# Optimization experiments

Hardware: AMD Instinct MI355X
Metric: run time of the kernel (lower is better)

## Reference

```python
import jax, jax.numpy as jnp
import numpy as np

V, C, H, W, RM, RD = 16, 16, 1024, 1024, 8, 4


def _cpx(x):
    # last dim 2 = (real, imag) -> complex64
    return jax.lax.complex(x[..., 0], x[..., 1])


def setup_inputs() -> dict:
    key = jax.random.key(0)
    ks = jax.random.split(key, 12)
    rn = lambda k, s, sc=1.0: jax.random.normal(k, s, dtype=jnp.float32) * sc
    ASYM = 0.01
    exp_init = jnp.array([2.0, 0.0], dtype=jnp.float32)  # exponents_initial_value_(real,imag)
    return {
        "base": rn(ks[0], (H, W, 2)),
        "mod_u": rn(ks[1], (C, H, RM, 2), 0.35),
        "mod_v": rn(ks[2], (C, RM, W, 2), 0.35),
        "del_u": rn(ks[3], (C, H, RD, 2), 0.35),
        "del_v": rn(ks[4], (C, RD, W, 2), 0.35),
        "exp_base": exp_init + rn(ks[5], (2,), ASYM),
        "exp_mod": exp_init[None, :] + rn(ks[6], (C, 2), ASYM),
        "exp_del": exp_init[None, :] + rn(ks[7], (C, 2), ASYM),
        "bias": rn(ks[8], (C, 2)),
        "scale": rn(ks[9], (C, 2)),
        "coef": rn(ks[10], (V, C, 2)),  # uniform(-2,2) real + small imag in torch; randn ok for baseline
    }


def reference(base, mod_u, mod_v, del_u, del_v, exp_base, exp_mod, exp_del, bias, scale, coef):
    b = _cpx(base)  # [H, W] complex64
    # low-rank complex reconstructions: [C, H, W]
    mod = jnp.einsum('chr,crw->chw', _cpx(mod_u), _cpx(mod_v))
    dlt = jnp.einsum('chr,crw->chw', _cpx(del_u), _cpx(del_v))
    # trainable complex exponentiation: z**w = exp(w * log z)
    pb = jnp.exp(_cpx(exp_base) * jnp.log(b))                        # [H, W]
    pm = jnp.exp(_cpx(exp_mod)[:, None, None] * jnp.log(mod))       # [C, H, W]
    pd = jnp.exp(_cpx(exp_del)[:, None, None] * jnp.log(dlt))       # [C, H, W]
    comp = _cpx(scale)[:, None, None] * (pb[None] * pm + pd) + _cpx(bias)[:, None, None]
    # coefficient-weighted sum over C components -> [V, H, W] (avoids [V,C,H,W] materialization)
    out = jnp.einsum('vc,chw->vhw', _cpx(coef), comp)
    return jnp.stack([out.real, out.imag], axis=-1)  # [V, H, W, 2] float32
```

## Files before the change

kernel.cpp:

```cpp
#include <hip/hip_runtime.h>
#include <stdint.h>

#define NV 16
#define NC 16
#define NH 1024
#define NW 1024
#define NRM 8
#define NRD 4

typedef __attribute__((ext_vector_type(4))) _Float16 f16x4;
typedef __attribute__((ext_vector_type(2))) __fp16 fp16x2_raw;
typedef __attribute__((ext_vector_type(4))) float f32x4;

#define MFMA16(a, b, c) __builtin_amdgcn_mfma_f32_16x16x16f16((a), (b), (c), 0, 0, 0)

struct cfloat { float x, y; };

__device__ __forceinline__ uint32_t pkh(float a, float b) {
    fp16x2_raw h = __builtin_amdgcn_cvt_pkrtz(a, b);
    return __builtin_bit_cast(uint32_t, h);
}

__device__ __forceinline__ f16x4 mk4(uint32_t lo, uint32_t hi) {
    union { uint32_t u[2]; f16x4 v; } t;
    t.u[0] = lo; t.u[1] = hi;
    return t.v;
}

__device__ __forceinline__ float fast_atan2f(float y, float x) {
    float ax = fabsf(x), ay = fabsf(y);
    float mx = fmaxf(ax, ay), mn = fminf(ax, ay);
    float a = __fdividef(mn, mx);
    float s = a * a;
    float p =              -0.01172120f;
    p = fmaf(p, s,  0.05265332f);
    p = fmaf(p, s, -0.11643287f);
    p = fmaf(p, s,  0.19354346f);
    p = fmaf(p, s, -0.33262347f);
    p = fmaf(p, s,  0.99997726f);
    p = p * a;
    float t = (ay > ax) ? (1.57079632679f - p) : p;
    t = (x < 0.0f) ? (3.14159265359f - t) : t;
    return (y < 0.0f) ? -t : t;
}

__device__ __forceinline__ cfloat cpow_(float zr, float zi, float wr, float wi) {
    float L  = 0.5f * __logf(fmaf(zr, zr, zi * zi));
    float th = fast_atan2f(zi, zr);
    float er = fmaf(wr, L,  -wi * th);
    float ei = fmaf(wr, th,  wi * L);
    float m  = __expf(er);
    float sv, cv;
    __sincosf(ei, &sv, &cv);
    cfloat r; r.x = m * cv; r.y = m * sv; return r;
}

#define CMAC(AR, AI, BR, BI) do { \
    tr_ = fmaf((AR), (BR), fmaf(-(AI), (BI), tr_)); \
    ti_ = fmaf((AR), (BI), fmaf( (AI), (BR), ti_)); } while (0)

__global__ __launch_bounds__(256)
void transpose_v(const float* __restrict__ mod_v, const float* __restrict__ del_v,
                 float* __restrict__ mvT, float* __restrict__ dvT)
{
    const int idx = blockIdx.x * 256 + threadIdx.x;
    const int c = idx >> 10, w = idx & 1023;
    float2* mt = reinterpret_cast<float2*>(mvT) + idx * NRM;
    const float2* ms = reinterpret_cast<const float2*>(mod_v) + c * NRM * NW + w;
    #pragma unroll
    for (int r = 0; r < NRM; ++r) mt[r] = ms[r * NW];
    float2* dt = reinterpret_cast<float2*>(dvT) + idx * NRD;
    const float2* dsrc = reinterpret_cast<const float2*>(del_v) + c * NRD * NW + w;
    #pragma unroll
    for (int r = 0; r < NRD; ++r) dt[r] = dsrc[r * NW];
}

struct V6 { float4 m0, m1, m2, m3, d0, d1; };

template <bool TR>
__device__ __forceinline__ V6 load_v(const float* __restrict__ mvT, const float* __restrict__ dvT,
                                     const float* __restrict__ mod_v, const float* __restrict__ del_v,
                                     int c, int w)
{
    V6 r;
    if (TR) {
        const float4* mp = reinterpret_cast<const float4*>(mvT) + (c * NW + w) * 4;
        r.m0 = mp[0]; r.m1 = mp[1]; r.m2 = mp[2]; r.m3 = mp[3];
        const float4* dp = reinterpret_cast<const float4*>(dvT) + (c * NW + w) * 2;
        r.d0 = dp[0]; r.d1 = dp[1];
    } else {
        const float2* m = reinterpret_cast<const float2*>(mod_v) + c * NRM * NW + w;
        float2 a0 = m[0], a1 = m[NW], a2 = m[2*NW], a3 = m[3*NW];
        float2 a4 = m[4*NW], a5 = m[5*NW], a6 = m[6*NW], a7 = m[7*NW];
        r.m0 = make_float4(a0.x, a0.y, a1.x, a1.y);
        r.m1 = make_float4(a2.x, a2.y, a3.x, a3.y);
        r.m2 = make_float4(a4.x, a4.y, a5.x, a5.y);
        r.m3 = make_float4(a6.x, a6.y, a7.x, a7.y);
        const float2* d = reinterpret_cast<const float2*>(del_v) + c * NRD * NW + w;
        float2 b0 = d[0], b1 = d[NW], b2 = d[2*NW], b3 = d[3*NW];
        r.d0 = make_float4(b0.x, b0.y, b1.x, b1.y);
        r.d1 = make_float4(b2.x, b2.y, b3.x, b3.y);
    }
    return r;
}

template <bool TR>
__global__ __launch_bounds__(256)
void fused_kernel(const float* __restrict__ base, const float* __restrict__ mod_u,
                  const float* __restrict__ mod_v, const float* __restrict__ del_u,
                  const float* __restrict__ del_v, const float* __restrict__ exp_base,
                  const float* __restrict__ exp_mod, const float* __restrict__ exp_del,
                  const float* __restrict__ bias_, const float* __restrict__ scale_,
                  const float* __restrict__ coef, float* __restrict__ out,
                  const float* __restrict__ mvT, const float* __restrict__ dvT)
{
    __shared__ uint32_t lds[8192];
    __shared__ float4 uA4[NC][2][4];
    __shared__ float4 uD4[NC][2][2];

    const int tid    = threadIdx.x;
    const int lane   = tid & 63;
    const int wv     = tid >> 6;
    const int wchunk = (int)(blockIdx.x & 3);
    const int hp     = (int)(blockIdx.x >> 2);
    const int w      = (wchunk << 8) | tid;
    const int h0     = hp * 2;
    const int wbase  = (wchunk << 8) | (wv << 6);

    {
        float* uAf = reinterpret_cast<float*>(uA4);
        float* uDf = reinterpret_cast<float*>(uD4);
        int i = tid;
        {
            const int c = i >> 5, rr = (i >> 4) & 1, e = i & 15;
            uAf[i] = mod_u[((c * NH) + (h0 + rr)) * (NRM * 2) + e];
        }
        i = tid + 256;
        {
            const int c = i >> 5, rr = (i >> 4) & 1, e = i & 15;
            uAf[i] = mod_u[((c * NH) + (h0 + rr)) * (NRM * 2) + e];
        }
        if (tid < 256) {
            const int c = tid >> 4, rr = (tid >> 3) & 1, e = tid & 7;
            uDf[tid] = del_u[((c * NH) + (h0 + rr)) * (NRD * 2) + e];
        }
    }
    __syncthreads();

    const int vv = lane & 15;
    const int c0 = (lane >> 4) << 2;

    const float4 cfa = *reinterpret_cast<const float4*>(coef   + (vv * NC + c0) * 2);
    const float4 cfb = *reinterpret_cast<const float4*>(coef   + (vv * NC + c0) * 2 + 4);
    const float4 sca = *reinterpret_cast<const float4*>(scale_ + c0 * 2);
    const float4 scb = *reinterpret_cast<const float4*>(scale_ + c0 * 2 + 4);
    const float4 bia = *reinterpret_cast<const float4*>(bias_  + c0 * 2);
    const float4 bib = *reinterpret_cast<const float4*>(bias_  + c0 * 2 + 4);

    float c2r0 = cfa.x*sca.x - cfa.y*sca.y, c2i0 = cfa.x*sca.y + cfa.y*sca.x;
    float c2r1 = cfa.z*sca.z - cfa.w*sca.w, c2i1 = cfa.z*sca.w + cfa.w*sca.z;
    float c2r2 = cfb.x*scb.x - cfb.y*scb.y, c2i2 = cfb.x*scb.y + cfb.y*scb.x;
    float c2r3 = cfb.z*scb.z - cfb.w*scb.w, c2i3 = cfb.z*scb.w + cfb.w*scb.z;

    const f16x4 Ar = mk4(pkh(c2r0, c2r1), pkh(c2r2, c2r3));
    const f16x4 Ai = mk4(pkh(c2i0, c2i1), pkh(c2i2, c2i3));
    const f16x4 An = mk4(pkh(-c2i0, -c2i1), pkh(-c2i2, -c2i3));

    const f16x4 Kr = mk4(pkh(cfa.x, cfa.z), pkh(cfb.x, cfb.z));
    const f16x4 Ki = mk4(pkh(cfa.y, cfa.w), pkh(cfb.y, cfb.w));
    const f16x4 Kn = mk4(pkh(-cfa.y, -cfa.w), pkh(-cfb.y, -cfb.w));

    const f16x4 Bbr = mk4(pkh(bia.x, bia.z), pkh(bib.x, bib.z));
    const f16x4 Bbi = mk4(pkh(bia.y, bia.w), pkh(bib.y, bib.w));

    const f32x4 zero4 = {0.f, 0.f, 0.f, 0.f};
    const f32x4 cr4 = MFMA16(Kr, Bbr, MFMA16(Kn, Bbi, zero4));
    const f32x4 ci4 = MFMA16(Ki, Bbr, MFMA16(Kr, Bbi, zero4));

    const float ebr = exp_base[0], ebi = exp_base[1];
    const float2 b0 = reinterpret_cast<const float2*>(base)[(h0    ) * NW + w];
    const float2 b1 = reinterpret_cast<const float2*>(base)[(h0 + 1) * NW + w];
    const cfloat pb0 = cpow_(b0.x, b0.y, ebr, ebi);
    const cfloat pb1 = cpow_(b1.x, b1.y, ebr, ebi);

    uint32_t* wlds0 = lds + (wv << 10);
    uint32_t* wlds1 = lds + 4096 + (wv << 10);
    const int swz_w = (lane >> 1) & 3;

    V6 cur = load_v<TR>(mvT, dvT, mod_v, del_v, 0, w);

    #pragma unroll 1
    for (int a = 0; a < 4; ++a) {
        uint32_t p0[4], p1[4];
        #pragma unroll
        for (int j = 0; j < 4; ++j) {
            const int c = (a << 2) | j;
            V6 nxt = load_v<TR>(mvT, dvT, mod_v, del_v, (c + 1) & 15, w);

            const float emr = exp_mod[2*c], emi = exp_mod[2*c+1];
            const float edr = exp_del[2*c], edi = exp_del[2*c+1];

            #pragma unroll
            for (int rr = 0; rr < 2; ++rr) {
                const float4 ua  = uA4[c][rr][0];
                const float4 ub  = uA4[c][rr][1];
                const float4 uc_ = uA4[c][rr][2];
                const float4 ud  = uA4[c][rr][3];
                const float4 da  = uD4[c][rr][0];
                const float4 db  = uD4[c][rr][1];

                float tr_ = 0.f, ti_ = 0.f;
                CMAC(ua.x,  ua.y,  cur.m0.x, cur.m0.y);
                CMAC(ua.z,  ua.w,  cur.m0.z, cur.m0.w);
                CMAC(ub.x,  ub.y,  cur.m1.x, cur.m1.y);
                CMAC(ub.z,  ub.w,  cur.m1.z, cur.m1.w);
                CMAC(uc_.x, uc_.y, cur.m2.x, cur.m2.y);
                CMAC(uc_.z, uc_.w, cur.m2.z, cur.m2.w);
                CMAC(ud.x,  ud.y,  cur.m3.x, cur.m3.y);
                CMAC(ud.z,  ud.w,  cur.m3.z, cur.m3.w);
                const float mr = tr_, mi_ = ti_;

                tr_ = 0.f; ti_ = 0.f;
                CMAC(da.x, da.y, cur.d0.x, cur.d0.y);
                CMAC(da.z, da.w, cur.d0.z, cur.d0.w);
                CMAC(db.x, db.y, cur.d1.x, cur.d1.y);
                CMAC(db.z, db.w, cur.d1.z, cur.d1.w);
                const float dr = tr_, di = ti_;

                const cfloat pm = cpow_(mr, mi_, emr, emi);
                const cfloat pd = cpow_(dr, di,  edr, edi);

                const float pbr = rr ? pb1.x : pb0.x;
                const float pbi = rr ? pb1.y : pb0.y;
                const float Pr = fmaf(pbr, pm.x, fmaf(-pbi, pm.y, pd.x));
                const float Pi = fmaf(pbr, pm.y, fmaf( pbi, pm.x, pd.y));
                const uint32_t pk = pkh(Pr, Pi);
                if (rr == 0) p0[j] = pk; else p1[j] = pk;
            }
            cur = nxt;
        }
        const int s = (a ^ swz_w) << 2;
        *reinterpret_cast<uint4*>(wlds0 + (lane << 4) + s) = make_uint4(p0[0], p0[1], p0[2], p0[3]);
        *reinterpret_cast<uint4*>(wlds1 + (lane << 4) + s) = make_uint4(p1[0], p1[1], p1[2], p1[3]);
    }

    const int ar  = lane >> 4;
    const int col = lane & 15;
    float2* outp = reinterpret_cast<float2*>(out);

    #pragma unroll
    for (int rr = 0; rr < 2; ++rr) {
        const uint32_t* reg = rr ? wlds1 : wlds0;
        const int h = h0 + rr;
        #pragma unroll
        for (int g = 0; g < 4; ++g) {
            const int p = (g << 4) | col;
            const int s = (ar ^ ((p >> 1) & 3)) << 2;
            const uint4 q = *reinterpret_cast<const uint4*>(reg + (p << 4) + s);
            const f16x4 Brf = mk4(__builtin_amdgcn_perm(q.y, q.x, 0x05040100u),
                                  __builtin_amdgcn_perm(q.w, q.z, 0x05040100u));
            const f16x4 Bif = mk4(__builtin_amdgcn_perm(q.y, q.x, 0x07060302u),
                                  __builtin_amdgcn_perm(q.w, q.z, 0x07060302u));
            const f32x4 Dr = MFMA16(Ar, Brf, MFMA16(An, Bif, cr4));
            const f32x4 Di = MFMA16(Ai, Brf, MFMA16(Ar, Bif, ci4));
            const int wg = wbase + (g << 4) + col;
            const int base_idx = h * NW + wg;
            #pragma unroll
            for (int j = 0; j < 4; ++j) {
                const int v = (ar << 2) + j;
                outp[v * (NH * NW) + base_idx] = make_float2(Dr[j], Di[j]);
            }
        }
    }
}

extern "C" void kernel_launch(void* const* d_in, const int* in_sizes, int n_in,
                              void* d_out, int out_size, void* d_ws, size_t ws_size,
                              hipStream_t stream) {
    const float* base     = (const float*)d_in[0];
    const float* mod_u    = (const float*)d_in[1];
    const float* mod_v    = (const float*)d_in[2];
    const float* del_u    = (const float*)d_in[3];
    const float* del_v    = (const float*)d_in[4];
    const float* exp_base = (const float*)d_in[5];
    const float* exp_mod  = (const float*)d_in[6];
    const float* exp_del  = (const float*)d_in[7];
    const float* bias_    = (const float*)d_in[8];
    const float* scale_   = (const float*)d_in[9];
    const float* coef     = (const float*)d_in[10];
    float* outp = (float*)d_out;

    const int blocks = (NH / 2) * (NW / 256);
    const size_t mvT_floats = (size_t)NC * NW * NRM * 2;
    const size_t dvT_floats = (size_t)NC * NW * NRD * 2;
    const size_t need = (mvT_floats + dvT_floats) * sizeof(float);

    if (ws_size >= need) {
        float* mvT = (float*)d_ws;
        float* dvT = mvT + mvT_floats;
        transpose_v<<<(NC * NW) / 256, 256, 0, stream>>>(mod_v, del_v, mvT, dvT);
        fused_kernel<true><<<blocks, 256, 0, stream>>>(base, mod_u, mod_v, del_u, del_v,
                                                       exp_base, exp_mod, exp_del,
                                                       bias_, scale_, coef, outp, mvT, dvT);
    } else {
        fused_kernel<false><<<blocks, 256, 0, stream>>>(base, mod_u, mod_v, del_u, del_v,
                                                        exp_base, exp_mod, exp_del,
                                                        bias_, scale_, coef, outp,
                                                        (const float*)nullptr, (const float*)nullptr);
    }
}
```

Before: 103.9 us.

## Compute complex powers in log2/revolution units with hardware transcendentals and fold base power

Rewrites the complex power evaluation to work in base-2 logarithm and revolution units, so the raw hardware log2, exp2, fract, sin and cos instructions can be used without range-reduction scaling. The atan2 polynomial is rescaled to return revolutions, and the per-component exponent constants are precomputed into shared memory. The base power is folded into the modulation exponent as an additive log term, removing one complex multiply and a separate exp/sincos per pixel. This reduces transcendental and ALU instruction count in the hot loop, at the cost of relying on the accuracy of the hardware approximations.

```diff
diff --git a/kernel.cpp b/kernel.cpp
--- a/kernel.cpp
+++ b/kernel.cpp
@@ -14,8 +14,6 @@
 
 #define MFMA16(a, b, c) __builtin_amdgcn_mfma_f32_16x16x16f16((a), (b), (c), 0, 0, 0)
 
-struct cfloat { float x, y; };
-
 __device__ __forceinline__ uint32_t pkh(float a, float b) {
     fp16x2_raw h = __builtin_amdgcn_cvt_pkrtz(a, b);
     return __builtin_bit_cast(uint32_t, h);
@@ -27,33 +25,25 @@
     return t.v;
 }
 
-__device__ __forceinline__ float fast_atan2f(float y, float x) {
+__device__ __forceinline__ float atan2_rev(float y, float x) {
     float ax = fabsf(x), ay = fabsf(y);
     float mx = fmaxf(ax, ay), mn = fminf(ax, ay);
-    float a = __fdividef(mn, mx);
+    float a = mn * __builtin_amdgcn_rcpf(mx);
     float s = a * a;
-    float p =              -0.01172120f;
-    p = fmaf(p, s,  0.05265332f);
-    p = fmaf(p, s, -0.11643287f);
-    p = fmaf(p, s,  0.19354346f);
-    p = fmaf(p, s, -0.33262347f);
-    p = fmaf(p, s,  0.99997726f);
+    float p =              -0.00186549f;
+    p = fmaf(p, s,  0.00838003f);
+    p = fmaf(p, s, -0.01852970f);
+    p = fmaf(p, s,  0.03080340f);
+    p = fmaf(p, s, -0.05294381f);
+    p = fmaf(p, s,  0.15915132f);
     p = p * a;
-    float t = (ay > ax) ? (1.57079632679f - p) : p;
-    t = (x < 0.0f) ? (3.14159265359f - t) : t;
+    float t = (ay > ax) ? (0.25f - p) : p;
+    t = (x < 0.0f) ? (0.5f - t) : t;
     return (y < 0.0f) ? -t : t;
 }
 
-__device__ __forceinline__ cfloat cpow_(float zr, float zi, float wr, float wi) {
-    float L  = 0.5f * __logf(fmaf(zr, zr, zi * zi));
-    float th = fast_atan2f(zi, zr);
-    float er = fmaf(wr, L,  -wi * th);
-    float ei = fmaf(wr, th,  wi * L);
-    float m  = __expf(er);
-    float sv, cv;
-    __sincosf(ei, &sv, &cv);
-    cfloat r; r.x = m * cv; r.y = m * sv; return r;
-}
+#define K_B 9.06472028f
+#define K_D 0.05516054f
 
 #define CMAC(AR, AI, BR, BI) do { \
     tr_ = fmaf((AR), (BR), fmaf(-(AI), (BI), tr_)); \
@@ -117,6 +107,7 @@
     __shared__ uint32_t lds[8192];
     __shared__ float4 uA4[NC][2][4];
     __shared__ float4 uD4[NC][2][2];
+    __shared__ float4 ctab[NC][2];
 
     const int tid    = threadIdx.x;
     const int lane   = tid & 63;
@@ -144,6 +135,12 @@
             const int c = tid >> 4, rr = (tid >> 3) & 1, e = tid & 7;
             uDf[tid] = del_u[((c * NH) + (h0 + rr)) * (NRD * 2) + e];
         }
+        if (tid < 32) {
+            const int c = tid >> 1, which = tid & 1;
+            const float* ep = which ? exp_del : exp_mod;
+            const float wr = ep[2*c], wi = ep[2*c+1];
+            ctab[c][which] = make_float4(0.5f * wr, wi * K_B, wr, wi * K_D);
+        }
     }
     __syncthreads();
 
@@ -178,10 +175,20 @@
     const f32x4 ci4 = MFMA16(Ki, Bbr, MFMA16(Kr, Bbi, zero4));
 
     const float ebr = exp_base[0], ebi = exp_base[1];
-    const float2 b0 = reinterpret_cast<const float2*>(base)[(h0    ) * NW + w];
-    const float2 b1 = reinterpret_cast<const float2*>(base)[(h0 + 1) * NW + w];
-    const cfloat pb0 = cpow_(b0.x, b0.y, ebr, ebi);
-    const cfloat pb1 = cpow_(b1.x, b1.y, ebr, ebi);
+    const float Ab = 0.5f * ebr, Bb = ebi * K_B, Cb = ebr, Db = ebi * K_D;
+    float berr[2], beir[2];
+    {
+        const float2 b0 = reinterpret_cast<const float2*>(base)[(h0    ) * NW + w];
+        const float2 b1 = reinterpret_cast<const float2*>(base)[(h0 + 1) * NW + w];
+        const float L2b0 = __builtin_amdgcn_logf(fmaf(b0.x, b0.x, b0.y * b0.y));
+        const float th0  = atan2_rev(b0.y, b0.x);
+        const float L2b1 = __builtin_amdgcn_logf(fmaf(b1.x, b1.x, b1.y * b1.y));
+        const float th1  = atan2_rev(b1.y, b1.x);
+        berr[0] = fmaf(Ab, L2b0, -Bb * th0);
+        beir[0] = fmaf(Cb, th0,   Db * L2b0);
+        berr[1] = fmaf(Ab, L2b1, -Bb * th1);
+        beir[1] = fmaf(Cb, th1,   Db * L2b1);
+    }
 
     uint32_t* wlds0 = lds + (wv << 10);
     uint32_t* wlds1 = lds + 4096 + (wv << 10);
@@ -197,8 +204,8 @@
             const int c = (a << 2) | j;
             V6 nxt = load_v<TR>(mvT, dvT, mod_v, del_v, (c + 1) & 15, w);
 
-            const float emr = exp_mod[2*c], emi = exp_mod[2*c+1];
-            const float edr = exp_del[2*c], edi = exp_del[2*c+1];
+            const float4 km = ctab[c][0];
+            const float4 kd = ctab[c][1];
 
             #pragma unroll
             for (int rr = 0; rr < 2; ++rr) {
@@ -227,13 +234,26 @@
                 CMAC(db.z, db.w, cur.d1.z, cur.d1.w);
                 const float dr = tr_, di = ti_;
 
-                const cfloat pm = cpow_(mr, mi_, emr, emi);
-                const cfloat pd = cpow_(dr, di,  edr, edi);
-
-                const float pbr = rr ? pb1.x : pb0.x;
-                const float pbi = rr ? pb1.y : pb0.y;
-                const float Pr = fmaf(pbr, pm.x, fmaf(-pbi, pm.y, pd.x));
-                const float Pi = fmaf(pbr, pm.y, fmaf( pbi, pm.x, pd.y));
+                const float L2m = __builtin_amdgcn_logf(fmaf(mr, mr, mi_ * mi_));
+                const float thm = atan2_rev(mi_, mr);
+                const float er2 = fmaf(km.x, L2m, fmaf(-km.y, thm, berr[rr]));
+                const float eir = fmaf(km.z, thm, fmaf(km.w, L2m, beir[rr]));
+                const float mm  = __builtin_amdgcn_exp2f(er2);
+                const float fm  = __builtin_amdgcn_fractf(eir);
+                const float cv  = __builtin_amdgcn_cosf(fm);
+                const float sv  = __builtin_amdgcn_sinf(fm);
+
+                const float L2d = __builtin_amdgcn_logf(fmaf(dr, dr, di * di));
+                const float thd = atan2_rev(di, dr);
+                const float er2d = fmaf(kd.x, L2d, -kd.y * thd);
+                const float eird = fmaf(kd.z, thd,  kd.w * L2d);
+                const float md  = __builtin_amdgcn_exp2f(er2d);
+                const float fd  = __builtin_amdgcn_fractf(eird);
+                const float cvd = __builtin_amdgcn_cosf(fd);
+                const float svd = __builtin_amdgcn_sinf(fd);
+
+                const float Pr = fmaf(mm, cv, md * cvd);
+                const float Pi = fmaf(mm, sv, md * svd);
                 const uint32_t pk = pkh(Pr, Pi);
                 if (rr == 0) p0[j] = pk; else p1[j] = pk;
             }
```

Result: slower. 110.4 us (+6.3%).
